# Kernel tuning notes

Hardware: AMD Instinct MI355X
Metric: run time of the kernel (lower is better)

The kernel has to match this reference:

```python
import jax, jax.numpy as jnp
import numpy as np

NEG_SLOPE = 0.2


def _gat_layer(x, src, dst, W, att_src, att_dst, bias, heads, out_c, concat):
    # x: [N, F_in]; src,dst: [E] (edges src -> dst, softmax grouped by dst)
    N = x.shape[0]
    h = (x @ W).reshape(N, heads, out_c)                       # [N,H,C]
    a_s = jnp.sum(h * att_src, axis=-1)                        # [N,H]
    a_d = jnp.sum(h * att_dst, axis=-1)                        # [N,H]
    e = jax.nn.leaky_relu(a_s[src] + a_d[dst], NEG_SLOPE)      # [E,H]
    emax = jax.ops.segment_max(e, dst, num_segments=N)         # [N,H]
    ex = jnp.exp(e - emax[dst])
    denom = jax.ops.segment_sum(ex, dst, num_segments=N)       # [N,H]
    alpha = ex / (denom[dst] + 1e-16)                          # [E,H]
    msg = h[src] * alpha[:, :, None]                           # [E,H,C]
    out = jax.ops.segment_sum(msg, dst, num_segments=N)        # [N,H,C]
    out = out.reshape(N, heads * out_c) if concat else out.mean(axis=1)
    return out + bias


def setup_inputs() -> dict:
    key = jax.random.key(0)
    ks = jax.random.split(key, 12)
    N, E = 100000, 1600000
    F_in, C1, H = 128, 32, 4
    x = jax.random.normal(ks[0], (N, F_in), dtype=jnp.float32)
    edge_index = jax.random.randint(ks[1], (2, E), 0, N, dtype=jnp.int64)
    s = 0.1
    W1 = jax.random.normal(ks[2], (F_in, H * C1), dtype=jnp.float32) * s
    att_src1 = jax.random.normal(ks[3], (H, C1), dtype=jnp.float32) * s
    att_dst1 = jax.random.normal(ks[4], (H, C1), dtype=jnp.float32) * s
    b1 = jnp.zeros((H * C1,), dtype=jnp.float32)
    W2 = jax.random.normal(ks[5], (H * C1, 1), dtype=jnp.float32) * s
    att_src2 = jax.random.normal(ks[6], (1, 1), dtype=jnp.float32) * s
    att_dst2 = jax.random.normal(ks[7], (1, 1), dtype=jnp.float32) * s
    b2 = jnp.zeros((1,), dtype=jnp.float32)
    return {"x": x, "edge_index": edge_index, "W1": W1, "att_src1": att_src1,
            "att_dst1": att_dst1, "b1": b1, "W2": W2, "att_src2": att_src2,
            "att_dst2": att_dst2, "b2": b2}


def reference(x, edge_index, W1, att_src1, att_dst1, b1, W2, att_src2, att_dst2, b2):
    N = x.shape[0]
    # PyG GATConv adds self loops by default
    loops = jnp.arange(N, dtype=edge_index.dtype)
    src = jnp.concatenate([edge_index[0], loops])
    dst = jnp.concatenate([edge_index[1], loops])
    h = _gat_layer(x, src, dst, W1, att_src1, att_dst1, b1, heads=4, out_c=32, concat=True)
    h = jax.nn.relu(h)
    out = _gat_layer(h, src, dst, W2, att_src2, att_dst2, b2, heads=1, out_c=1, concat=False)
    return out.squeeze(-1)  # [N]
```

## Files before the change

### kernel.cpp

```cpp
#include <hip/hip_runtime.h>
#include <hip/hip_bf16.h>
#include <math.h>

typedef __hip_bfloat16 bf16;
typedef __attribute__((ext_vector_type(8))) short short8v;
typedef __attribute__((ext_vector_type(4))) float float4v;

__device__ __forceinline__ float b2f(bf16 v) { return __bfloat162float(v); }
__device__ __forceinline__ float bs2f(unsigned short s) {
    unsigned u = ((unsigned)s) << 16;
    float f; __builtin_memcpy(&f, &u, 4); return f;
}
__device__ __forceinline__ short f2bs(float v) {
    bf16 b = __float2bfloat16(v);
    short s; __builtin_memcpy(&s, &b, 2); return s;
}
__device__ __forceinline__ float lrelu(float v) { return v > 0.f ? v : 0.2f * v; }
__device__ __forceinline__ float ldf(const void* p, size_t i, int bf) {
    return bf ? b2f(((const bf16*)p)[i]) : ((const float*)p)[i];
}
__device__ __forceinline__ int ld_src(const int* ei, int e, int E, int f64, int N) {
    int v = f64 ? (int)(((const long long*)ei)[e]) : ei[e];
    if ((unsigned)v >= (unsigned)N) v = 0;
    return v;
}
__device__ __forceinline__ int ld_dst(const int* ei, int e, int E, int f64, int N) {
    int v = f64 ? (int)(((const long long*)ei)[(size_t)E + e]) : ei[(size_t)E + e];
    if ((unsigned)v >= (unsigned)N) v = 0;
    return v;
}

#define EPB 4096
#define SB  8

__global__ void k_detect(const int* __restrict__ ei, const unsigned* __restrict__ xw,
                         int* __restrict__ flags)
{
    __shared__ int s_or[256];
    __shared__ int s_cnt[256];
    int t = threadIdx.x;
    int any = 0, cnt = 0;
    for (int i = t; i < 4096; i += 256) {
        any |= ei[2 * i + 1];
        unsigned e = (xw[i] >> 7) & 0xFFu;
        cnt += (e >= 100u && e <= 134u) ? 1 : 0;
    }
    s_or[t] = any; s_cnt[t] = cnt;
    __syncthreads();
    for (int s = 128; s > 0; s >>= 1) {
        if (t < s) { s_or[t] |= s_or[t + s]; s_cnt[t] += s_cnt[t + s]; }
        __syncthreads();
    }
    if (t == 0) {
        flags[0] = (s_or[0] == 0) ? 1 : 0;
        flags[1] = (s_cnt[0] > 2048) ? 1 : 0;
    }
}

__global__ void k_zero(int* __restrict__ p, int n)
{
    int i = blockIdx.x * blockDim.x + threadIdx.x;
    if (i < n) p[i] = 0;
}

__global__ void k_w1frag(const void* __restrict__ W1, const int* __restrict__ flags,
                         short* __restrict__ w1frag)
{
    int bf = flags[1];
    int idx = blockIdx.x * 256 + threadIdx.x;
    if (idx >= 16384) return;
    int j = idx & 7, l = (idx >> 3) & 63, kk = (idx >> 9) & 3, ct = idx >> 11;
    int k = kk * 32 + (l >> 4) * 8 + j;
    int n = ct * 16 + (l & 15);
    w1frag[idx] = bf ? ((const short*)W1)[k * 128 + n]
                     : f2bs(((const float*)W1)[k * 128 + n]);
}

__global__ void __launch_bounds__(256)
k_bbin_count(const int* __restrict__ ei, const int* __restrict__ flags,
             int* __restrict__ bcnt, int E, int N, int nbuck)
{
    __shared__ int hist[512];
    int t = threadIdx.x;
    for (int j = t; j < nbuck; j += 256) hist[j] = 0;
    __syncthreads();
    int f = flags[0];
    int beg = blockIdx.x * EPB, end = min(E, beg + EPB);
    for (int i = beg + t; i < end; i += 256)
        atomicAdd(&hist[ld_dst(ei, i, E, f, N) >> SB], 1);
    __syncthreads();
    for (int j = t; j < nbuck; j += 256)
        if (hist[j]) atomicAdd(&bcnt[j], hist[j]);
}

__global__ void __launch_bounds__(512)
k_bscan(const int* __restrict__ bcnt, int* __restrict__ bofs,
        int* __restrict__ bcur, int* __restrict__ offsets,
        int nbuck, int E, int N)
{
    __shared__ int sh[512];
    int t = threadIdx.x;
    int v = (t < nbuck) ? bcnt[t] : 0;
    sh[t] = v;
    __syncthreads();
    for (int s = 1; s < 512; s <<= 1) {
        int add = (t >= s) ? sh[t - s] : 0;
        __syncthreads();
        sh[t] += add;
        __syncthreads();
    }
    if (t < nbuck) { bofs[t] = sh[t] - v; bcur[t] = sh[t] - v; }
    if (t == 0) { bofs[nbuck] = E; offsets[N] = E; }
}

__global__ void __launch_bounds__(256)
k_bbin_scatter(const int* __restrict__ ei, const int* __restrict__ flags,
               int* __restrict__ bcur, uint2* __restrict__ ebuf,
               int E, int N, int nbuck)
{
    __shared__ int hist[512];
    __shared__ int base[512];
    int t = threadIdx.x;
    for (int j = t; j < nbuck; j += 256) hist[j] = 0;
    __syncthreads();
    int f = flags[0];
    int beg = blockIdx.x * EPB, end = min(E, beg + EPB);
    for (int i = beg + t; i < end; i += 256)
        atomicAdd(&hist[ld_dst(ei, i, E, f, N) >> SB], 1);
    __syncthreads();
    for (int j = t; j < nbuck; j += 256) {
        base[j] = hist[j] ? atomicAdd(&bcur[j], hist[j]) : 0;
        hist[j] = 0;
    }
    __syncthreads();
    for (int i = beg + t; i < end; i += 256) {
        int d = ld_dst(ei, i, E, f, N);
        int s = ld_src(ei, i, E, f, N);
        int b = d >> SB;
        int idx = base[b] + atomicAdd(&hist[b], 1);
        ebuf[idx] = make_uint2((unsigned)s, (unsigned)d);
    }
}

__global__ void __launch_bounds__(256)
k_bucket_csr(const uint2* __restrict__ ebuf, const int* __restrict__ bofs,
             int* __restrict__ offsets, int* __restrict__ adj, int N)
{
    const int npb = 1 << SB;
    __shared__ int hist[npb];
    __shared__ int psum[256];
    int b = blockIdx.x, t = threadIdx.x;
    int n0 = b << SB;
    int ebeg = bofs[b], eend = bofs[b + 1];

    hist[t] = 0;
    __syncthreads();
    for (int i = ebeg + t; i < eend; i += 256)
        atomicAdd(&hist[ebuf[i].y - n0], 1);
    __syncthreads();
    int c = hist[t];
    psum[t] = c;
    __syncthreads();
    for (int st = 1; st < 256; st <<= 1) {
        int add = (t >= st) ? psum[t - st] : 0;
        __syncthreads();
        psum[t] += add;
        __syncthreads();
    }
    int run = ebeg + psum[t] - c;
    int node = n0 + t;
    hist[t] = run;
    if (node < N) offsets[node] = run;
    __syncthreads();
    for (int i = ebeg + t; i < eend; i += 256) {
        uint2 e = ebuf[i];
        int pos = atomicAdd(&hist[e.y - n0], 1);
        adj[pos] = (int)e.x;
    }
}

#define GPS 132

__global__ void __launch_bounds__(256)
k_gemm2(const void* __restrict__ x, const short* __restrict__ w1frag,
        const void* __restrict__ att_src, const void* __restrict__ att_dst,
        const int* __restrict__ flags, bf16* __restrict__ h1b,
        float* __restrict__ a_s, float* __restrict__ a_d, int N)
{
    __shared__ short sm[4][16 * GPS];
    int bf = flags[1];
    int t = threadIdx.x, wv = t >> 6, l = t & 63, lq = l >> 4, lr = l & 15;
    int m0 = blockIdx.x * 64 + wv * 16;

    int arow = m0 + lr;
    if (arow >= N) arow = N - 1;
    short8v afr[4];
    if (bf) {
        const unsigned short* xp = (const unsigned short*)x + (size_t)arow * 128;
#pragma unroll
        for (int kk = 0; kk < 4; ++kk)
            afr[kk] = *(const short8v*)(xp + kk * 32 + lq * 8);
    } else {
        const float* xp = (const float*)x + (size_t)arow * 128;
#pragma unroll
        for (int kk = 0; kk < 4; ++kk) {
            float4 f0 = *(const float4*)(xp + kk * 32 + lq * 8);
            float4 f1 = *(const float4*)(xp + kk * 32 + lq * 8 + 4);
            short8v a;
            a[0] = f2bs(f0.x); a[1] = f2bs(f0.y); a[2] = f2bs(f0.z); a[3] = f2bs(f0.w);
            a[4] = f2bs(f1.x); a[5] = f2bs(f1.y); a[6] = f2bs(f1.z); a[7] = f2bs(f1.w);
            afr[kk] = a;
        }
    }

    float4v acc[8];
#pragma unroll
    for (int ct = 0; ct < 8; ++ct) acc[ct] = (float4v){0.f, 0.f, 0.f, 0.f};

#pragma unroll
    for (int kk = 0; kk < 4; ++kk) {
        short8v a = afr[kk];
#pragma unroll
        for (int ct = 0; ct < 8; ++ct) {
            short8v b = *(const short8v*)(w1frag + (((ct * 4 + kk) * 64 + l) << 3));
            acc[ct] = __builtin_amdgcn_mfma_f32_16x16x32_bf16(a, b, acc[ct], 0, 0, 0);
        }
    }

#pragma unroll
    for (int ct = 0; ct < 8; ++ct)
#pragma unroll
        for (int r = 0; r < 4; ++r)
            sm[wv][(lq * 4 + r) * GPS + ct * 16 + lr] = f2bs(acc[ct][r]);
    __syncthreads();

    int c0 = (l & 7) * 16;
    float asv[16], adv[16];
#pragma unroll
    for (int c = 0; c < 16; ++c) {
        asv[c] = ldf(att_src, c0 + c, bf);
        adv[c] = ldf(att_dst, c0 + c, bf);
    }
#pragma unroll
    for (int p = 0; p < 2; ++p) {
        int rrow = p * 8 + (l >> 3);
        int gn = m0 + rrow;
        const short* srcp = &sm[wv][rrow * GPS + c0];
        short8v v0 = *(const short8v*)srcp;
        short8v v1 = *(const short8v*)(srcp + 8);
        if (gn < N) {
            unsigned short* dst = (unsigned short*)h1b + (size_t)gn * 128 + c0;
            *(short8v*)dst = v0;
            *(short8v*)(dst + 8) = v1;
        }
        float ds = 0.f, dd = 0.f;
#pragma unroll
        for (int c = 0; c < 8; ++c) {
            float fv = bs2f((unsigned short)v0[c]);
            ds += fv * asv[c]; dd += fv * adv[c];
        }
#pragma unroll
        for (int c = 0; c < 8; ++c) {
            float fv = bs2f((unsigned short)v1[c]);
            ds += fv * asv[8 + c]; dd += fv * adv[8 + c];
        }
        ds += __shfl_xor(ds, 1, 64);
        dd += __shfl_xor(dd, 1, 64);
        if (gn < N && ((l & 1) == 0)) {
            int h = (l & 7) >> 1;
            a_s[(size_t)gn * 4 + h] = ds;
            a_d[(size_t)gn * 4 + h] = dd;
        }
    }
}

__global__ void __launch_bounds__(256)
k_hagg32(const bf16* __restrict__ h1b, const float* __restrict__ a_s,
         const float* __restrict__ a_d, const int* __restrict__ offsets,
         const int* __restrict__ adj, const void* __restrict__ b1,
         const void* __restrict__ W2, const int* __restrict__ flags,
         float* __restrict__ h2, int N)
{
    int bf = flags[1];
    int t = threadIdx.x;
    int g = t >> 5, l = t & 31;
    int n = blockIdx.x * 8 + g;
    if (n >= N) return;
    int h = l >> 3;
    int coff = h * 32 + (l & 7) * 4;

    int beg = offsets[n], deg = offsets[n + 1] - beg;
    float adh = a_d[(size_t)n * 4 + h];
    const unsigned short* h1u = (const unsigned short*)h1b;

    float wself = __expf(lrelu(a_s[(size_t)n * 4 + h] + adh));
    ushort4 u = *(const ushort4*)(h1u + ((size_t)n << 7) + coff);
    float a0 = wself * bs2f(u.x), a1 = wself * bs2f(u.y);
    float a2 = wself * bs2f(u.z), a3 = wself * bs2f(u.w);
    float den = wself;

    int i = 0;
    for (; i + 2 <= deg; i += 2) {
        int s0 = adj[beg + i];
        int s1 = adj[beg + i + 1];
        float w0 = __expf(lrelu(a_s[(size_t)s0 * 4 + h] + adh));
        float w1 = __expf(lrelu(a_s[(size_t)s1 * 4 + h] + adh));
        ushort4 v0 = *(const ushort4*)(h1u + ((size_t)s0 << 7) + coff);
        ushort4 v1 = *(const ushort4*)(h1u + ((size_t)s1 << 7) + coff);
        den += w0 + w1;
        a0 += w0 * bs2f(v0.x) + w1 * bs2f(v1.x);
        a1 += w0 * bs2f(v0.y) + w1 * bs2f(v1.y);
        a2 += w0 * bs2f(v0.z) + w1 * bs2f(v1.z);
        a3 += w0 * bs2f(v0.w) + w1 * bs2f(v1.w);
    }
    if (i < deg) {
        int s0 = adj[beg + i];
        float w0 = __expf(lrelu(a_s[(size_t)s0 * 4 + h] + adh));
        ushort4 v0 = *(const ushort4*)(h1u + ((size_t)s0 << 7) + coff);
        den += w0;
        a0 += w0 * bs2f(v0.x);
        a1 += w0 * bs2f(v0.y);
        a2 += w0 * bs2f(v0.z);
        a3 += w0 * bs2f(v0.w);
    }

    float inv = 1.f / (den + 1e-16f);
    float o0 = fmaxf(a0 * inv + ldf(b1, coff + 0, bf), 0.f);
    float o1 = fmaxf(a1 * inv + ldf(b1, coff + 1, bf), 0.f);
    float o2 = fmaxf(a2 * inv + ldf(b1, coff + 2, bf), 0.f);
    float o3 = fmaxf(a3 * inv + ldf(b1, coff + 3, bf), 0.f);

    float p = o0 * ldf(W2, coff + 0, bf) + o1 * ldf(W2, coff + 1, bf)
            + o2 * ldf(W2, coff + 2, bf) + o3 * ldf(W2, coff + 3, bf);
    p += __shfl_xor(p, 1, 64);
    p += __shfl_xor(p, 2, 64);
    p += __shfl_xor(p, 4, 64);
    p += __shfl_xor(p, 8, 64);
    p += __shfl_xor(p, 16, 64);
    if (l == 0) h2[n] = p;
}

__global__ void k_agg2(const float* __restrict__ h2, const int* __restrict__ offsets,
                       const int* __restrict__ adj, const void* __restrict__ att_src2,
                       const void* __restrict__ att_dst2, const void* __restrict__ bias2,
                       const int* __restrict__ flags, void* __restrict__ out, int N)
{
    int bf = flags[1];
    int g = (blockIdx.x * blockDim.x + threadIdx.x) >> 4;
    int lane = threadIdx.x & 15;
    if (g >= N) return;
    int n = g;
    float as2 = ldf(att_src2, 0, bf), ad2 = ldf(att_dst2, 0, bf);
    int beg = offsets[n], end = offsets[n + 1], deg = end - beg;
    float hn = h2[n];
    float dterm = hn * ad2;

    float acc = 0.f, den = 0.f;
    if (lane == 0) {
        float ex = __expf(lrelu(hn * as2 + dterm));
        acc = ex * hn; den = ex;
    }
    for (int i = lane; i < deg; i += 16) {
        int s = adj[beg + i];
        float hs = h2[s];
        float ex = __expf(lrelu(hs * as2 + dterm));
        acc += ex * hs; den += ex;
    }
    for (int m = 1; m < 16; m <<= 1) {
        acc += __shfl_xor(acc, m, 64);
        den += __shfl_xor(den, m, 64);
    }
    if (lane == 0) {
        float r = acc / (den + 1e-16f) + ldf(bias2, 0, bf);
        if (bf) ((bf16*)out)[n] = __float2bfloat16(r);
        else    ((float*)out)[n] = r;
    }
}

extern "C" void kernel_launch(void* const* d_in, const int* in_sizes, int n_in,
                              void* d_out, int out_size, void* d_ws, size_t ws_size,
                              hipStream_t stream)
{
    const void* x        = d_in[0];
    const int*  ei       = (const int*)d_in[1];
    const void* W1       = d_in[2];
    const void* att_src1 = d_in[3];
    const void* att_dst1 = d_in[4];
    const void* b1       = d_in[5];
    const void* W2       = d_in[6];
    const void* att_src2 = d_in[7];
    const void* att_dst2 = d_in[8];
    const void* bias2    = d_in[9];

    int N = in_sizes[0] / 128;
    int E = in_sizes[1] / 2;
    int nbuck = ((N - 1) >> SB) + 1;

    char* ws = (char*)d_ws;
    size_t off = 0;
    auto alloc = [&](size_t bytes) -> void* {
        void* p = ws + off;
        off = (off + bytes + 255) & ~(size_t)255;
        return p;
    };
    int*   flags   = (int*)alloc(256);
    float* a_s     = (float*)alloc((size_t)N * 4 * sizeof(float));
    float* a_d     = (float*)alloc((size_t)N * 4 * sizeof(float));
    float* h2      = (float*)alloc((size_t)N * sizeof(float));
    int*   offsets = (int*)alloc((size_t)(N + 1) * sizeof(int));
    int*   adj     = (int*)alloc((size_t)E * sizeof(int));
    uint2* ebuf    = (uint2*)alloc((size_t)E * sizeof(uint2));
    int*   bcnt    = (int*)alloc(1024 * sizeof(int));
    int*   bofs    = (int*)alloc(1028 * sizeof(int));
    int*   bcur    = (int*)alloc(1024 * sizeof(int));
    short* w1frag  = (short*)alloc(16384 * sizeof(short));
    bf16*  h1b     = (bf16*)alloc((size_t)N * 128 * sizeof(bf16));

    k_detect<<<1, 256, 0, stream>>>(ei, (const unsigned*)x, flags);
    k_zero<<<(nbuck + 255) / 256, 256, 0, stream>>>(bcnt, nbuck);
    k_w1frag<<<64, 256, 0, stream>>>(W1, flags, w1frag);

    int ebl = (E + EPB - 1) / EPB;
    k_bbin_count<<<ebl, 256, 0, stream>>>(ei, flags, bcnt, E, N, nbuck);
    k_bscan<<<1, 512, 0, stream>>>(bcnt, bofs, bcur, offsets, nbuck, E, N);
    k_bbin_scatter<<<ebl, 256, 0, stream>>>(ei, flags, bcur, ebuf, E, N, nbuck);
    k_bucket_csr<<<nbuck, 256, 0, stream>>>(ebuf, bofs, offsets, adj, N);

    k_gemm2<<<(N + 63) / 64, 256, 0, stream>>>(x, w1frag, att_src1, att_dst1,
                                               flags, h1b, a_s, a_d, N);

    k_hagg32<<<(N + 7) / 8, 256, 0, stream>>>(h1b, a_s, a_d, offsets, adj,
                                              b1, W2, flags, h2, N);

    k_agg2<<<((size_t)N * 16 + 255) / 256, 256, 0, stream>>>(
        h2, offsets, adj, att_src2, att_dst2, bias2, flags, d_out, N);
}
```

Measured before the change: 289.6 us.

## Merge setup kernels, fold bucket scan into GEMM launch, unroll aggregation

Removes three kernel launches: bucket zeroing moves into k_detect, W1 fragment packing joins the bucket-count kernel as extra blocks, and the bucket prefix scan runs as block 0 of the GEMM kernel. The GEMM now stages a 64-row x tile through LDS with coalesced loads instead of per-lane strided global reads. The layer-1 aggregation loop is unrolled from 2 to 4 edges to keep more gathers in flight. The cost is larger shared memory in the GEMM, which may lower occupancy, and more register pressure in the aggregation loop.

New measurement: 279.9 us. 3.3% less time.

```diff
diff --git a/kernel.cpp b/kernel.cpp
--- a/kernel.cpp
+++ b/kernel.cpp
@@ -34,11 +34,12 @@
 #define SB  8
 
 __global__ void k_detect(const int* __restrict__ ei, const unsigned* __restrict__ xw,
-                         int* __restrict__ flags)
+                         int* __restrict__ flags, int* __restrict__ bcnt, int nbuck)
 {
     __shared__ int s_or[256];
     __shared__ int s_cnt[256];
     int t = threadIdx.x;
+    for (int j = t; j < nbuck; j += 256) bcnt[j] = 0;
     int any = 0, cnt = 0;
     for (int i = t; i < 4096; i += 256) {
         any |= ei[2 * i + 1];
@@ -57,31 +58,25 @@
     }
 }
 
-__global__ void k_zero(int* __restrict__ p, int n)
-{
-    int i = blockIdx.x * blockDim.x + threadIdx.x;
-    if (i < n) p[i] = 0;
-}
-
-__global__ void k_w1frag(const void* __restrict__ W1, const int* __restrict__ flags,
-                         short* __restrict__ w1frag)
-{
-    int bf = flags[1];
-    int idx = blockIdx.x * 256 + threadIdx.x;
-    if (idx >= 16384) return;
-    int j = idx & 7, l = (idx >> 3) & 63, kk = (idx >> 9) & 3, ct = idx >> 11;
-    int k = kk * 32 + (l >> 4) * 8 + j;
-    int n = ct * 16 + (l & 15);
-    w1frag[idx] = bf ? ((const short*)W1)[k * 128 + n]
-                     : f2bs(((const float*)W1)[k * 128 + n]);
-}
-
 __global__ void __launch_bounds__(256)
-k_bbin_count(const int* __restrict__ ei, const int* __restrict__ flags,
-             int* __restrict__ bcnt, int E, int N, int nbuck)
-{
+k_prep(const int* __restrict__ ei, const void* __restrict__ W1,
+       const int* __restrict__ flags, int* __restrict__ bcnt,
+       short* __restrict__ w1frag, int E, int N, int nbuck, int ebl)
+{
+    int t = threadIdx.x;
+    if (blockIdx.x >= ebl) {
+        int bf = flags[1];
+        int idx = (blockIdx.x - ebl) * 256 + t;
+        if (idx < 16384) {
+            int j = idx & 7, l = (idx >> 3) & 63, kk = (idx >> 9) & 3, ct = idx >> 11;
+            int k = kk * 32 + (l >> 4) * 8 + j;
+            int n = ct * 16 + (l & 15);
+            w1frag[idx] = bf ? ((const short*)W1)[k * 128 + n]
+                             : f2bs(((const float*)W1)[k * 128 + n]);
+        }
+        return;
+    }
     __shared__ int hist[512];
-    int t = threadIdx.x;
     for (int j = t; j < nbuck; j += 256) hist[j] = 0;
     __syncthreads();
     int f = flags[0];
@@ -93,24 +88,132 @@
         if (hist[j]) atomicAdd(&bcnt[j], hist[j]);
 }
 
-__global__ void __launch_bounds__(512)
-k_bscan(const int* __restrict__ bcnt, int* __restrict__ bofs,
-        int* __restrict__ bcur, int* __restrict__ offsets,
-        int nbuck, int E, int N)
-{
-    __shared__ int sh[512];
+#define GP 136
+
+__global__ void __launch_bounds__(256)
+k_gemm_scan(const void* __restrict__ x, const short* __restrict__ w1frag,
+            const void* __restrict__ att_src, const void* __restrict__ att_dst,
+            const int* __restrict__ flags, bf16* __restrict__ h1b,
+            float* __restrict__ a_s, float* __restrict__ a_d,
+            const int* __restrict__ bcnt, int* __restrict__ bofs,
+            int* __restrict__ bcur, int* __restrict__ offsets,
+            int N, int E, int nbuck)
+{
     int t = threadIdx.x;
-    int v = (t < nbuck) ? bcnt[t] : 0;
-    sh[t] = v;
-    __syncthreads();
-    for (int s = 1; s < 512; s <<= 1) {
-        int add = (t >= s) ? sh[t - s] : 0;
+    if (blockIdx.x == 0) {
+        __shared__ int ps[256];
+        int i0 = 2 * t, i1 = 2 * t + 1;
+        int c0 = (i0 < nbuck) ? bcnt[i0] : 0;
+        int c1 = (i1 < nbuck) ? bcnt[i1] : 0;
+        int pr = c0 + c1;
+        ps[t] = pr;
         __syncthreads();
-        sh[t] += add;
-        __syncthreads();
-    }
-    if (t < nbuck) { bofs[t] = sh[t] - v; bcur[t] = sh[t] - v; }
-    if (t == 0) { bofs[nbuck] = E; offsets[N] = E; }
+        for (int s = 1; s < 256; s <<= 1) {
+            int add = (t >= s) ? ps[t - s] : 0;
+            __syncthreads();
+            ps[t] += add;
+            __syncthreads();
+        }
+        int excl = ps[t] - pr;
+        if (i0 < nbuck) { bofs[i0] = excl; bcur[i0] = excl; }
+        if (i1 < nbuck) { bofs[i1] = excl + c0; bcur[i1] = excl + c0; }
+        if (t == 0) { bofs[nbuck] = E; offsets[N] = E; }
+        return;
+    }
+    __shared__ short xs[64 * GP];
+    int bf = flags[1];
+    int blk = blockIdx.x - 1;
+    int base = blk * 64;
+    if (bf) {
+        const short8v* xp = (const short8v*)x;
+        for (int idx = t; idx < 1024; idx += 256) {
+            int m = idx >> 4, v8 = idx & 15;
+            int gm = base + m;
+            short8v v = (gm < N) ? xp[(size_t)gm * 16 + v8]
+                                 : (short8v){0,0,0,0,0,0,0,0};
+            *(short8v*)&xs[m * GP + v8 * 8] = v;
+        }
+    } else {
+        const float4* xp = (const float4*)x;
+        for (int idx = t; idx < 2048; idx += 256) {
+            int m = idx >> 5, v4 = idx & 31;
+            int gm = base + m;
+            float4 f = (gm < N) ? xp[(size_t)gm * 32 + v4]
+                                : make_float4(0.f, 0.f, 0.f, 0.f);
+            short* d = &xs[m * GP + v4 * 4];
+            d[0] = f2bs(f.x); d[1] = f2bs(f.y); d[2] = f2bs(f.z); d[3] = f2bs(f.w);
+        }
+    }
+    __syncthreads();
+
+    int wv = t >> 6, l = t & 63, lq = l >> 4, lr = l & 15;
+    int m0 = base + wv * 16;
+
+    short8v afr[4];
+#pragma unroll
+    for (int kk = 0; kk < 4; ++kk)
+        afr[kk] = *(const short8v*)&xs[(wv * 16 + lr) * GP + kk * 32 + lq * 8];
+
+    float4v acc[8];
+#pragma unroll
+    for (int ct = 0; ct < 8; ++ct) acc[ct] = (float4v){0.f, 0.f, 0.f, 0.f};
+
+#pragma unroll
+    for (int kk = 0; kk < 4; ++kk) {
+        short8v a = afr[kk];
+#pragma unroll
+        for (int ct = 0; ct < 8; ++ct) {
+            short8v b = *(const short8v*)(w1frag + (((ct * 4 + kk) * 64 + l) << 3));
+            acc[ct] = __builtin_amdgcn_mfma_f32_16x16x32_bf16(a, b, acc[ct], 0, 0, 0);
+        }
+    }
+    __syncthreads();
+
+#pragma unroll
+    for (int ct = 0; ct < 8; ++ct)
+#pragma unroll
+        for (int r = 0; r < 4; ++r)
+            xs[(wv * 16 + lq * 4 + r) * GP + ct * 16 + lr] = f2bs(acc[ct][r]);
+    __syncthreads();
+
+    int c0 = (l & 7) * 16;
+    float asv[16], adv[16];
+#pragma unroll
+    for (int c = 0; c < 16; ++c) {
+        asv[c] = ldf(att_src, c0 + c, bf);
+        adv[c] = ldf(att_dst, c0 + c, bf);
+    }
+#pragma unroll
+    for (int p = 0; p < 2; ++p) {
+        int rrow = p * 8 + (l >> 3);
+        int gn = m0 + rrow;
+        const short* srcp = &xs[(wv * 16 + rrow) * GP + c0];
+        short8v v0 = *(const short8v*)srcp;
+        short8v v1 = *(const short8v*)(srcp + 8);
+        if (gn < N) {
+            unsigned short* dst = (unsigned short*)h1b + (size_t)gn * 128 + c0;
+            *(short8v*)dst = v0;
+            *(short8v*)(dst + 8) = v1;
+        }
+        float ds = 0.f, dd = 0.f;
+#pragma unroll
+        for (int c = 0; c < 8; ++c) {
+            float fv = bs2f((unsigned short)v0[c]);
+            ds += fv * asv[c]; dd += fv * adv[c];
+        }
+#pragma unroll
+        for (int c = 0; c < 8; ++c) {
+            float fv = bs2f((unsigned short)v1[c]);
+            ds += fv * asv[8 + c]; dd += fv * adv[8 + c];
+        }
+        ds += __shfl_xor(ds, 1, 64);
+        dd += __shfl_xor(dd, 1, 64);
+        if (gn < N && ((l & 1) == 0)) {
+            int h = (l & 7) >> 1;
+            a_s[(size_t)gn * 4 + h] = ds;
+            a_d[(size_t)gn * 4 + h] = dd;
+        }
+    }
 }
 
 __global__ void __launch_bounds__(256)
@@ -176,101 +279,6 @@
         uint2 e = ebuf[i];
         int pos = atomicAdd(&hist[e.y - n0], 1);
         adj[pos] = (int)e.x;
-    }
-}
-
-#define GPS 132
-
-__global__ void __launch_bounds__(256)
-k_gemm2(const void* __restrict__ x, const short* __restrict__ w1frag,
-        const void* __restrict__ att_src, const void* __restrict__ att_dst,
-        const int* __restrict__ flags, bf16* __restrict__ h1b,
-        float* __restrict__ a_s, float* __restrict__ a_d, int N)
-{
-    __shared__ short sm[4][16 * GPS];
-    int bf = flags[1];
-    int t = threadIdx.x, wv = t >> 6, l = t & 63, lq = l >> 4, lr = l & 15;
-    int m0 = blockIdx.x * 64 + wv * 16;
-
-    int arow = m0 + lr;
-    if (arow >= N) arow = N - 1;
-    short8v afr[4];
-    if (bf) {
-        const unsigned short* xp = (const unsigned short*)x + (size_t)arow * 128;
-#pragma unroll
-        for (int kk = 0; kk < 4; ++kk)
-            afr[kk] = *(const short8v*)(xp + kk * 32 + lq * 8);
-    } else {
-        const float* xp = (const float*)x + (size_t)arow * 128;
-#pragma unroll
-        for (int kk = 0; kk < 4; ++kk) {
-            float4 f0 = *(const float4*)(xp + kk * 32 + lq * 8);
-            float4 f1 = *(const float4*)(xp + kk * 32 + lq * 8 + 4);
-            short8v a;
-            a[0] = f2bs(f0.x); a[1] = f2bs(f0.y); a[2] = f2bs(f0.z); a[3] = f2bs(f0.w);
-            a[4] = f2bs(f1.x); a[5] = f2bs(f1.y); a[6] = f2bs(f1.z); a[7] = f2bs(f1.w);
-            afr[kk] = a;
-        }
-    }
-
-    float4v acc[8];
-#pragma unroll
-    for (int ct = 0; ct < 8; ++ct) acc[ct] = (float4v){0.f, 0.f, 0.f, 0.f};
-
-#pragma unroll
-    for (int kk = 0; kk < 4; ++kk) {
-        short8v a = afr[kk];
-#pragma unroll
-        for (int ct = 0; ct < 8; ++ct) {
-            short8v b = *(const short8v*)(w1frag + (((ct * 4 + kk) * 64 + l) << 3));
-            acc[ct] = __builtin_amdgcn_mfma_f32_16x16x32_bf16(a, b, acc[ct], 0, 0, 0);
-        }
-    }
-
-#pragma unroll
-    for (int ct = 0; ct < 8; ++ct)
-#pragma unroll
-        for (int r = 0; r < 4; ++r)
-            sm[wv][(lq * 4 + r) * GPS + ct * 16 + lr] = f2bs(acc[ct][r]);
-    __syncthreads();
-
-    int c0 = (l & 7) * 16;
-    float asv[16], adv[16];
-#pragma unroll
-    for (int c = 0; c < 16; ++c) {
-        asv[c] = ldf(att_src, c0 + c, bf);
-        adv[c] = ldf(att_dst, c0 + c, bf);
-    }
-#pragma unroll
-    for (int p = 0; p < 2; ++p) {
-        int rrow = p * 8 + (l >> 3);
-        int gn = m0 + rrow;
-        const short* srcp = &sm[wv][rrow * GPS + c0];
-        short8v v0 = *(const short8v*)srcp;
-        short8v v1 = *(const short8v*)(srcp + 8);
-        if (gn < N) {
-            unsigned short* dst = (unsigned short*)h1b + (size_t)gn * 128 + c0;
-            *(short8v*)dst = v0;
-            *(short8v*)(dst + 8) = v1;
-        }
-        float ds = 0.f, dd = 0.f;
-#pragma unroll
-        for (int c = 0; c < 8; ++c) {
-            float fv = bs2f((unsigned short)v0[c]);
-            ds += fv * asv[c]; dd += fv * adv[c];
-        }
-#pragma unroll
-        for (int c = 0; c < 8; ++c) {
-            float fv = bs2f((unsigned short)v1[c]);
-            ds += fv * asv[8 + c]; dd += fv * adv[8 + c];
-        }
-        ds += __shfl_xor(ds, 1, 64);
-        dd += __shfl_xor(dd, 1, 64);
-        if (gn < N && ((l & 1) == 0)) {
-            int h = (l & 7) >> 1;
-            a_s[(size_t)gn * 4 + h] = ds;
-            a_d[(size_t)gn * 4 + h] = dd;
-        }
     }
 }
 
@@ -300,20 +308,26 @@
     float den = wself;
 
     int i = 0;
-    for (; i + 2 <= deg; i += 2) {
+    for (; i + 4 <= deg; i += 4) {
         int s0 = adj[beg + i];
         int s1 = adj[beg + i + 1];
+        int s2 = adj[beg + i + 2];
+        int s3 = adj[beg + i + 3];
         float w0 = __expf(lrelu(a_s[(size_t)s0 * 4 + h] + adh));
         float w1 = __expf(lrelu(a_s[(size_t)s1 * 4 + h] + adh));
+        float w2 = __expf(lrelu(a_s[(size_t)s2 * 4 + h] + adh));
+        float w3 = __expf(lrelu(a_s[(size_t)s3 * 4 + h] + adh));
         ushort4 v0 = *(const ushort4*)(h1u + ((size_t)s0 << 7) + coff);
         ushort4 v1 = *(const ushort4*)(h1u + ((size_t)s1 << 7) + coff);
-        den += w0 + w1;
-        a0 += w0 * bs2f(v0.x) + w1 * bs2f(v1.x);
-        a1 += w0 * bs2f(v0.y) + w1 * bs2f(v1.y);
-        a2 += w0 * bs2f(v0.z) + w1 * bs2f(v1.z);
-        a3 += w0 * bs2f(v0.w) + w1 * bs2f(v1.w);
-    }
-    if (i < deg) {
+        ushort4 v2 = *(const ushort4*)(h1u + ((size_t)s2 << 7) + coff);
+        ushort4 v3 = *(const ushort4*)(h1u + ((size_t)s3 << 7) + coff);
+        den += (w0 + w1) + (w2 + w3);
+        a0 += w0 * bs2f(v0.x) + w1 * bs2f(v1.x) + w2 * bs2f(v2.x) + w3 * bs2f(v3.x);
+        a1 += w0 * bs2f(v0.y) + w1 * bs2f(v1.y) + w2 * bs2f(v2.y) + w3 * bs2f(v3.y);
+        a2 += w0 * bs2f(v0.z) + w1 * bs2f(v1.z) + w2 * bs2f(v2.z) + w3 * bs2f(v3.z);
+        a3 += w0 * bs2f(v0.w) + w1 * bs2f(v1.w) + w2 * bs2f(v2.w) + w3 * bs2f(v3.w);
+    }
+    for (; i < deg; ++i) {
         int s0 = adj[beg + i];
         float w0 = __expf(lrelu(a_s[(size_t)s0 * 4 + h] + adh));
         ushort4 v0 = *(const ushort4*)(h1u + ((size_t)s0 << 7) + coff);
@@ -416,19 +430,20 @@
     short* w1frag  = (short*)alloc(16384 * sizeof(short));
     bf16*  h1b     = (bf16*)alloc((size_t)N * 128 * sizeof(bf16));
 
-    k_detect<<<1, 256, 0, stream>>>(ei, (const unsigned*)x, flags);
-    k_zero<<<(nbuck + 255) / 256, 256, 0, stream>>>(bcnt, nbuck);
-    k_w1frag<<<64, 256, 0, stream>>>(W1, flags, w1frag);
-
     int ebl = (E + EPB - 1) / EPB;
-    k_bbin_count<<<ebl, 256, 0, stream>>>(ei, flags, bcnt, E, N, nbuck);
-    k_bscan<<<1, 512, 0, stream>>>(bcnt, bofs, bcur, offsets, nbuck, E, N);
+
+    k_detect<<<1, 256, 0, stream>>>(ei, (const unsigned*)x, flags, bcnt, nbuck);
+
+    k_prep<<<ebl + 64, 256, 0, stream>>>(ei, W1, flags, bcnt, w1frag,
+                                         E, N, nbuck, ebl);
+
+    k_gemm_scan<<<1 + (N + 63) / 64, 256, 0, stream>>>(
+        x, w1frag, att_src1, att_dst1, flags, h1b, a_s, a_d,
+        bcnt, bofs, bcur, offsets, N, E, nbuck);
+
     k_bbin_scatter<<<ebl, 256, 0, stream>>>(ei, flags, bcur, ebuf, E, N, nbuck);
     k_bucket_csr<<<nbuck, 256, 0, stream>>>(ebuf, bofs, offsets, adj, N);
 
-    k_gemm2<<<(N + 63) / 64, 256, 0, stream>>>(x, w1frag, att_src1, att_dst1,
-                                               flags, h1b, a_s, a_d, N);
-
     k_hagg32<<<(N + 7) / 8, 256, 0, stream>>>(h1b, a_s, a_d, offsets, adj,
                                               b1, W2, flags, h2, N);
 
```
